# Performance work log

Hardware: AMD Instinct MI355X
Metric: run time of the kernel (lower is better)

The kernel has to match this reference:

```python
import jax, jax.numpy as jnp
import numpy as np

N_STREAMS = 4096


def setup_inputs() -> dict:
    key = jax.random.key(0)
    # Plain Gaussian (well-separated singular values; the polar factor math is
    # identical to the module's eye + 0.01*randn init, just a different point).
    H_raw = jax.random.normal(key, (N_STREAMS, N_STREAMS), dtype=jnp.float32)
    return {"H_raw": H_raw}


def reference(H_raw) -> jnp.ndarray:
    # OrthogonalMixing.forward: orthogonal polar factor of H_raw via thin SVD.
    U, s, Vh = jnp.linalg.svd(H_raw, full_matrices=False)
    return U @ Vh  # (s, s), satisfies H^T H = I
```

## Files before the change

kernel.cpp:

```cpp
#include <hip/hip_runtime.h>
#include <hip/hip_bf16.h>
#include <hip/hip_fp16.h>

#define NN 4096
#define NGROW 8
#define NPOL 2
#define NITER (NGROW + NPOL)
#define NPOW 12
#define NKT (NN / 64)
#define NTRI 136
#define PRESCALE 32.0f

using f16 = _Float16;
typedef __attribute__((ext_vector_type(4))) float f32x4;
typedef __attribute__((ext_vector_type(8))) f16 h16x8;

__device__ inline void gl_lds16(const void* g, void* l) {
  __builtin_amdgcn_global_load_lds(
      (const __attribute__((address_space(1))) unsigned int*)(unsigned long long)(uintptr_t)g,
      (__attribute__((address_space(3))) unsigned int*)(uintptr_t)l,
      16, 0, 0);
}

template <int EPI, int TRI>
__global__ __launch_bounds__(512, 2) void gemm_nt(
    const f16* __restrict__ P, const f16* __restrict__ Q,
    void* __restrict__ Out, const f16* __restrict__ aux,
    float alpha, float beta) {
  int bi, bj;
  if (TRI) {
    const int t = blockIdx.x;
    int r = (int)((sqrtf(8.0f * (float)t + 1.0f) - 1.0f) * 0.5f);
    while ((r + 1) * (r + 2) / 2 <= t) ++r;
    while (r * (r + 1) / 2 > t) --r;
    bi = r;
    bj = t - r * (r + 1) / 2;
  } else {
    bi = blockIdx.x;
    bj = blockIdx.y;
  }

  __shared__ f16 lA[2][256 * 64];
  __shared__ f16 lB[2][256 * 64];

  const int tid = threadIdx.x;
  const int lane = tid & 63;
  const int wv = tid >> 6;
  const int wr = wv >> 2;
  const int wc = wv & 3;
  const int m = lane & 15;
  const int qd = lane >> 4;
  const int srow = tid >> 3;
  const int schk = tid & 7;

  f32x4 acc[8][4] = {};

#define STAGE_A(u_, kk_, b_)                                                  \
  do {                                                                        \
    const int rr_ = (u_)*64 + srow;                                           \
    gl_lds16(P + (size_t)(bi * 256 + rr_) * NN + (kk_) + ((schk ^ (srow & 7)) * 8), \
             &lA[b_][(u_)*4096 + tid * 8]);                                   \
  } while (0)
#define STAGE_B(u_, kk_, b_)                                                  \
  do {                                                                        \
    const int rr_ = (u_)*64 + srow;                                           \
    gl_lds16(Q + (size_t)(bj * 256 + rr_) * NN + (kk_) + ((schk ^ (srow & 7)) * 8), \
             &lB[b_][(u_)*4096 + tid * 8]);                                   \
  } while (0)

#define READ_B_FR(b_)                                                         \
  do {                                                                        \
    _Pragma("unroll") for (int cf = 0; cf < 4; ++cf)                          \
    _Pragma("unroll") for (int ks = 0; ks < 2; ++ks) {                        \
      const int rb = wc * 64 + cf * 16 + m;                                   \
      const int cb = (ks * 4 + qd) ^ (rb & 7);                                \
      bv[cf][ks] = *(const h16x8*)&lB[b_][rb * 64 + cb * 8];                  \
    }                                                                         \
  } while (0)
#define READ_A_FR(b_, q_)                                                     \
  do {                                                                        \
    _Pragma("unroll") for (int rf = 0; rf < 2; ++rf)                          \
    _Pragma("unroll") for (int ks = 0; ks < 2; ++ks) {                        \
      const int ra = wr * 128 + (q_)*32 + rf * 16 + m;                        \
      const int ca = (ks * 4 + qd) ^ (ra & 7);                                \
      av[rf][ks] = *(const h16x8*)&lA[b_][ra * 64 + ca * 8];                  \
    }                                                                         \
  } while (0)
#define MFMA_Q(q_)                                                            \
  do {                                                                        \
    _Pragma("unroll") for (int rf = 0; rf < 2; ++rf)                          \
    _Pragma("unroll") for (int cf = 0; cf < 4; ++cf)                          \
    _Pragma("unroll") for (int ks = 0; ks < 2; ++ks)                          \
        acc[(q_)*2 + rf][cf] = __builtin_amdgcn_mfma_f32_16x16x32_f16(        \
            av[rf][ks], bv[cf][ks], acc[(q_)*2 + rf][cf], 0, 0, 0);           \
  } while (0)

#define BAR() __builtin_amdgcn_s_barrier()
#define PRIO(x_) __builtin_amdgcn_s_setprio(x_)
#define VMCNT(n_) asm volatile("s_waitcnt vmcnt(" #n_ ")" ::: "memory")
#define LGKM(n_) asm volatile("s_waitcnt lgkmcnt(" #n_ ")" ::: "memory")

#define TILE_STEADY(t_, b_, nb_)                                              \
  {                                                                           \
    const int k1 = ((t_) + 1) * 64, k2 = ((t_) + 2) * 64;                     \
    h16x8 av[2][2], bv[4][2];                                                 \
    READ_B_FR(b_);                                                            \
    READ_A_FR(b_, 0);                                                         \
    STAGE_A(1, k1, nb_); STAGE_A(3, k1, nb_);                                 \
    LGKM(8); BAR(); LGKM(0);                                                  \
    PRIO(1); MFMA_Q(0); PRIO(0);                                              \
    READ_A_FR(b_, 1);                                                         \
    STAGE_B(0, k2, b_); STAGE_B(1, k2, b_);                                   \
    BAR(); LGKM(0);                                                           \
    PRIO(1); MFMA_Q(1); PRIO(0);                                              \
    READ_A_FR(b_, 2);                                                         \
    STAGE_B(2, k2, b_); STAGE_B(3, k2, b_);                                   \
    BAR(); LGKM(0);                                                           \
    PRIO(1); MFMA_Q(2); PRIO(0);                                              \
    READ_A_FR(b_, 3);                                                         \
    STAGE_A(0, k2, b_); STAGE_A(2, k2, b_);                                   \
    BAR(); LGKM(0);                                                           \
    PRIO(1); MFMA_Q(3); PRIO(0);                                              \
    VMCNT(6); BAR();                                                          \
  }

  STAGE_B(0, 0, 0); STAGE_B(1, 0, 0); STAGE_B(2, 0, 0); STAGE_B(3, 0, 0);
  STAGE_A(0, 0, 0); STAGE_A(1, 0, 0); STAGE_A(2, 0, 0); STAGE_A(3, 0, 0);
  STAGE_B(0, 64, 1); STAGE_B(1, 64, 1); STAGE_B(2, 64, 1); STAGE_B(3, 64, 1);
  STAGE_A(0, 64, 1); STAGE_A(2, 64, 1);
  VMCNT(6);
  BAR();

  for (int tt = 0; tt < NKT - 2; tt += 2) {
    TILE_STEADY(tt, 0, 1);
    TILE_STEADY(tt + 1, 1, 0);
  }

  {
    h16x8 av[2][2], bv[4][2];
    READ_B_FR(0);
    READ_A_FR(0, 0);
    STAGE_A(1, (NKT - 1) * 64, 1); STAGE_A(3, (NKT - 1) * 64, 1);
    LGKM(8); BAR(); LGKM(0);
    PRIO(1); MFMA_Q(0); PRIO(0);
    READ_A_FR(0, 1);
    BAR(); LGKM(0);
    PRIO(1); MFMA_Q(1); PRIO(0);
    READ_A_FR(0, 2);
    BAR(); LGKM(0);
    PRIO(1); MFMA_Q(2); PRIO(0);
    READ_A_FR(0, 3);
    BAR(); LGKM(0);
    PRIO(1); MFMA_Q(3); PRIO(0);
    VMCNT(0); BAR();
  }
  {
    h16x8 av[2][2], bv[4][2];
    READ_B_FR(1);
    READ_A_FR(1, 0);
    LGKM(8); BAR(); LGKM(0);
    PRIO(1); MFMA_Q(0); PRIO(0);
    READ_A_FR(1, 1);
    BAR(); LGKM(0);
    PRIO(1); MFMA_Q(1); PRIO(0);
    READ_A_FR(1, 2);
    BAR(); LGKM(0);
    PRIO(1); MFMA_Q(2); PRIO(0);
    READ_A_FR(1, 3);
    BAR(); LGKM(0);
    PRIO(1); MFMA_Q(3); PRIO(0);
  }

#pragma unroll
  for (int fr = 0; fr < 8; ++fr) {
#pragma unroll
    for (int fc = 0; fc < 4; ++fc) {
#pragma unroll
      for (int rg = 0; rg < 4; ++rg) {
        const int lr = wr * 128 + fr * 16 + qd * 4 + rg;
        const int lc = wc * 64 + fc * 16 + m;
        const size_t idx = (size_t)(bi * 256 + lr) * NN + bj * 256 + lc;
        float v = beta * acc[fr][fc][rg];
        if (alpha != 0.0f) v += alpha * (float)aux[idx];
        if (EPI == 0)
          ((f16*)Out)[idx] = (f16)v;
        else
          ((float*)Out)[idx] = v;
        if (TRI && bi != bj) {
          const size_t idxT = (size_t)(bj * 256 + lc) * NN + bi * 256 + lr;
          ((f16*)Out)[idxT] = (f16)v;
        }
      }
    }
  }
#undef STAGE_A
#undef STAGE_B
#undef READ_B_FR
#undef READ_A_FR
#undef MFMA_Q
#undef TILE_STEADY
#undef BAR
#undef PRIO
#undef VMCNT
#undef LGKM
}

__global__ void transpose_h(const unsigned short* __restrict__ in,
                            unsigned short* __restrict__ out) {
  __shared__ unsigned short tile[64][65];
  const int tx = threadIdx.x & 63;
  const int ty = threadIdx.x >> 6;
  const int bx = blockIdx.x, by = blockIdx.y;
#pragma unroll
  for (int rr = 0; rr < 16; ++rr) {
    const int row = rr * 4 + ty;
    tile[row][tx] = in[(size_t)(by * 64 + row) * NN + bx * 64 + tx];
  }
  __syncthreads();
#pragma unroll
  for (int rr = 0; rr < 16; ++rr) {
    const int row = rr * 4 + ty;
    out[(size_t)(bx * 64 + row) * NN + by * 64 + tx] = tile[tx][row];
  }
}

__global__ __launch_bounds__(256) void powmv(const f16* __restrict__ A,
                                             const float* __restrict__ vin,
                                             const float* __restrict__ snin,
                                             float* __restrict__ vout,
                                             float* __restrict__ snout) {
  const float scale = rsqrtf(*snin);
  const int row = blockIdx.x * 4 + (threadIdx.x >> 6);
  const int lane = threadIdx.x & 63;
  const f16* arow = A + (size_t)row * NN;
  float acc = 0.0f;
#pragma unroll
  for (int p = 0; p < 8; ++p) {
    const int c = p * 512 + lane * 8;
    const h16x8 av = *(const h16x8*)(arow + c);
    const float4 w0 = *(const float4*)(vin + c);
    const float4 w1 = *(const float4*)(vin + c + 4);
    acc += (float)av[0] * w0.x + (float)av[1] * w0.y + (float)av[2] * w0.z +
           (float)av[3] * w0.w + (float)av[4] * w1.x + (float)av[5] * w1.y +
           (float)av[6] * w1.z + (float)av[7] * w1.w;
  }
  for (int off = 32; off; off >>= 1) acc += __shfl_down(acc, off, 64);
  if (lane == 0) {
    const float u = acc * scale;
    vout[row] = u;
    atomicAdd(snout, u * u);
  }
}

__global__ void init_pw(float* __restrict__ v0, float* __restrict__ slots) {
  const int t = threadIdx.x;
  if (t < 64) slots[t] = (t == 1) ? 1.0f : 0.0f;
  for (int i = t; i < NN; i += 256) {
    const unsigned h = (unsigned)i * 2654435761u;
    v0[i] = ((h >> 16) & 1) ? 0.015625f : -0.015625f;
  }
}

__global__ void reduce_sumsq(const float* __restrict__ h, float* __restrict__ slots) {
  float acc = 0.0f;
  const size_t total = (size_t)NN * NN;
  for (size_t i = (size_t)blockIdx.x * blockDim.x + threadIdx.x; i < total;
       i += (size_t)gridDim.x * blockDim.x) {
    const float v = h[i];
    acc += v * v;
  }
  for (int off = 32; off; off >>= 1) acc += __shfl_down(acc, off, 64);
  __shared__ float ws[4];
  const int lane = threadIdx.x & 63, wv = threadIdx.x >> 6;
  if (lane == 0) ws[wv] = acc;
  __syncthreads();
  if (threadIdx.x == 0) atomicAdd(&slots[0], ws[0] + ws[1] + ws[2] + ws[3]);
}

__global__ void scale_cast(const float* __restrict__ h, const float* __restrict__ slots,
                           f16* __restrict__ xb, int mode) {
  float inv = rsqrtf(slots[0]) * PRESCALE;
  if (mode) inv *= rsqrtf(1.10f * sqrtf(slots[1 + NPOW]));
  const size_t i = ((size_t)blockIdx.x * blockDim.x + threadIdx.x) * 4;
  const float4 v = *(const float4*)(h + i);
  union { f16 hh[4]; ushort4 u; } cvt;
  cvt.hh[0] = (f16)(v.x * inv);
  cvt.hh[1] = (f16)(v.y * inv);
  cvt.hh[2] = (f16)(v.z * inv);
  cvt.hh[3] = (f16)(v.w * inv);
  *(ushort4*)(xb + i) = cvt.u;
}

__global__ void rescale_f16(f16* __restrict__ a, const float* __restrict__ slots) {
  const float cA = 1.0f / (1.10f * sqrtf(slots[1 + NPOW]));
  const size_t i = ((size_t)blockIdx.x * 256 + threadIdx.x) * 8;
  h16x8 v = *(h16x8*)(a + i);
  h16x8 o;
#pragma unroll
  for (int j = 0; j < 8; ++j) o[j] = (f16)((float)v[j] * cA);
  *(h16x8*)(a + i) = o;
}

extern "C" void kernel_launch(void* const* d_in, const int* in_sizes, int n_in,
                              void* d_out, int out_size, void* d_ws, size_t ws_size,
                              hipStream_t stream) {
  (void)in_sizes; (void)n_in; (void)out_size; (void)ws_size;
  const float* H = (const float*)d_in[0];
  float* out = (float*)d_out;
  char* ws = (char*)d_ws;

  f16* P0 = (f16*)ws;
  f16* P1 = (f16*)(ws + ((size_t)32 << 20));
  f16* Ab = (f16*)(ws + ((size_t)64 << 20));
  f16* Bb = (f16*)((char*)d_out + ((size_t)32 << 20));
  float* v0 = (float*)d_out;
  float* v1 = (float*)((char*)d_out + 16384);
  float* slots = (float*)((char*)d_out + 32768);

  const dim3 gfull(16, 16), tbg(512), tb(256), gt(64, 64);

  init_pw<<<1, 256, 0, stream>>>(v0, slots);
  reduce_sumsq<<<1024, 256, 0, stream>>>(H, slots);
  scale_cast<<<(NN * (size_t)NN) / 4 / 256, 256, 0, stream>>>(H, slots, P0, 0);
  transpose_h<<<gt, tb, 0, stream>>>((const unsigned short*)P0, (unsigned short*)P1);
  gemm_nt<0, 1><<<NTRI, tbg, 0, stream>>>(P1, P1, Ab, (f16*)nullptr, 0.0f, 1.0f);
  for (int k = 0; k < NPOW; ++k) {
    const float* vi = (k & 1) ? v1 : v0;
    float* vo = (k & 1) ? v0 : v1;
    powmv<<<1024, 256, 0, stream>>>(Ab, vi, &slots[1 + k], vo, &slots[2 + k]);
  }
  rescale_f16<<<(NN * (size_t)NN) / 8 / 256, 256, 0, stream>>>(Ab, slots);
  scale_cast<<<(NN * (size_t)NN) / 4 / 256, 256, 0, stream>>>(H, slots, P0, 1);

  f16* X = P0;
  f16* Y = P1;
  const float GA = 3.4445f, GB = -4.7750f, GC = 2.0315f;
  const float PA = 1.875f, PB = -1.25f, PC = 0.375f;

  for (int it = 0; it < NITER; ++it) {
    const bool polish = it >= NGROW;
    const bool last = (it == NITER - 1);
    const float qa = polish ? PA : GA, qb = polish ? PB : GB, qc = polish ? PC : GC;

    if (it > 0) {
      transpose_h<<<gt, tb, 0, stream>>>((const unsigned short*)X, (unsigned short*)Y);
      gemm_nt<0, 1><<<NTRI, tbg, 0, stream>>>(Y, Y, Ab, (f16*)nullptr, 0.0f, 1.0f);
    }
    f16* Bdst = last ? Y : Bb;
    gemm_nt<0, 1><<<NTRI, tbg, 0, stream>>>(Ab, Ab, Bdst, Ab, qb, qc);
    if (!last) {
      gemm_nt<0, 0><<<gfull, tbg, 0, stream>>>(X, Bdst, Y, X, qa, 1.0f);
      f16* t = X; X = Y; Y = t;
    } else {
      gemm_nt<1, 0><<<gfull, tbg, 0, stream>>>(X, Bdst, out, X, qa, 1.0f);
    }
  }
}
```

Before: 4.708 ms.

## Software-pipeline LDS fragment reads with double-buffered registers and sched_group_barrier interleave

Restructures the GEMM main loop so the LDS fragment reads for the next quarter (and the next tile's B fragments) are issued while the current quarter's MFMAs run, using ping-pong register buffers for A and B. The explicit lgkmcnt waits and setprio calls are replaced by sched_group_barrier directives that interleave ds_reads, global-to-LDS loads and MFMAs. The goal is to hide LDS read latency behind matrix-core work instead of stalling before each MFMA block. In exchange it needs more VGPRs for the doubled fragment buffers, which may lower occupancy or cause spills, and it relies on the compiler honoring the schedule hints for correct waitcnt placement.

```diff
diff --git a/kernel.cpp b/kernel.cpp
--- a/kernel.cpp
+++ b/kernel.cpp
@@ -54,6 +54,8 @@
   const int schk = tid & 7;
 
   f32x4 acc[8][4] = {};
+  h16x8 avA[2][2], avB[2][2];
+  h16x8 bv0[4][2], bv1[4][2];
 
 #define STAGE_A(u_, kk_, b_)                                                  \
   do {                                                                        \
@@ -68,60 +70,77 @@
              &lB[b_][(u_)*4096 + tid * 8]);                                   \
   } while (0)
 
-#define READ_B_FR(b_)                                                         \
+#define READ_AV(dst_, b_, q_)                                                 \
+  do {                                                                        \
+    _Pragma("unroll") for (int rf = 0; rf < 2; ++rf)                          \
+    _Pragma("unroll") for (int ks = 0; ks < 2; ++ks) {                        \
+      const int ra = wr * 128 + (q_)*32 + rf * 16 + m;                        \
+      const int ca = (ks * 4 + qd) ^ (ra & 7);                                \
+      dst_[rf][ks] = *(const h16x8*)&lA[b_][ra * 64 + ca * 8];                \
+    }                                                                         \
+  } while (0)
+#define READ_BV(dst_, b_)                                                     \
   do {                                                                        \
     _Pragma("unroll") for (int cf = 0; cf < 4; ++cf)                          \
     _Pragma("unroll") for (int ks = 0; ks < 2; ++ks) {                        \
       const int rb = wc * 64 + cf * 16 + m;                                   \
       const int cb = (ks * 4 + qd) ^ (rb & 7);                                \
-      bv[cf][ks] = *(const h16x8*)&lB[b_][rb * 64 + cb * 8];                  \
+      dst_[cf][ks] = *(const h16x8*)&lB[b_][rb * 64 + cb * 8];                \
     }                                                                         \
   } while (0)
-#define READ_A_FR(b_, q_)                                                     \
-  do {                                                                        \
-    _Pragma("unroll") for (int rf = 0; rf < 2; ++rf)                          \
-    _Pragma("unroll") for (int ks = 0; ks < 2; ++ks) {                        \
-      const int ra = wr * 128 + (q_)*32 + rf * 16 + m;                        \
-      const int ca = (ks * 4 + qd) ^ (ra & 7);                                \
-      av[rf][ks] = *(const h16x8*)&lA[b_][ra * 64 + ca * 8];                  \
-    }                                                                         \
-  } while (0)
-#define MFMA_Q(q_)                                                            \
+#define MFMA_Q(q_, A_, B_)                                                    \
   do {                                                                        \
     _Pragma("unroll") for (int rf = 0; rf < 2; ++rf)                          \
     _Pragma("unroll") for (int cf = 0; cf < 4; ++cf)                          \
     _Pragma("unroll") for (int ks = 0; ks < 2; ++ks)                          \
         acc[(q_)*2 + rf][cf] = __builtin_amdgcn_mfma_f32_16x16x32_f16(        \
-            av[rf][ks], bv[cf][ks], acc[(q_)*2 + rf][cf], 0, 0, 0);           \
+            A_[rf][ks], B_[cf][ks], acc[(q_)*2 + rf][cf], 0, 0, 0);           \
   } while (0)
 
 #define BAR() __builtin_amdgcn_s_barrier()
-#define PRIO(x_) __builtin_amdgcn_s_setprio(x_)
 #define VMCNT(n_) asm volatile("s_waitcnt vmcnt(" #n_ ")" ::: "memory")
-#define LGKM(n_) asm volatile("s_waitcnt lgkmcnt(" #n_ ")" ::: "memory")
-
-#define TILE_STEADY(t_, b_, nb_)                                              \
+#define SGB(m_, n_) __builtin_amdgcn_sched_group_barrier(m_, n_, 0)
+#define SGB_RD4_ST2()                                                         \
+  do { SGB(0x8,2); SGB(0x100,1); SGB(0x8,2); SGB(0x100,1); SGB(0x8,2);        \
+       SGB(0x100,1); SGB(0x8,2); SGB(0x100,1); SGB(0x8,2); SGB(0x30,1);       \
+       SGB(0x8,3); SGB(0x30,1); SGB(0x8,3); } while (0)
+#define SGB_RD4_ST0()                                                         \
+  do { SGB(0x8,3); SGB(0x100,1); SGB(0x8,3); SGB(0x100,1); SGB(0x8,3);        \
+       SGB(0x100,1); SGB(0x8,3); SGB(0x100,1); SGB(0x8,4); } while (0)
+#define SGB_RD12_ST2()                                                        \
+  do { SGB(0x100,2); SGB(0x8,2); SGB(0x100,2); SGB(0x8,2); SGB(0x100,2);      \
+       SGB(0x8,2); SGB(0x100,2); SGB(0x8,2); SGB(0x100,2); SGB(0x8,2);        \
+       SGB(0x100,2); SGB(0x8,2); SGB(0x30,1); SGB(0x8,2); SGB(0x30,1);        \
+       SGB(0x8,2); } while (0)
+#define SGB_RD12_ST0()                                                        \
+  do { SGB(0x100,2); SGB(0x8,2); SGB(0x100,2); SGB(0x8,2); SGB(0x100,2);      \
+       SGB(0x8,2); SGB(0x100,2); SGB(0x8,2); SGB(0x100,2); SGB(0x8,2);        \
+       SGB(0x100,2); SGB(0x8,2); SGB(0x8,4); } while (0)
+
+#define TILE_STEADY(t_, b_, nb_, BVC_, BVN_)                                  \
   {                                                                           \
     const int k1 = ((t_) + 1) * 64, k2 = ((t_) + 2) * 64;                     \
-    h16x8 av[2][2], bv[4][2];                                                 \
-    READ_B_FR(b_);                                                            \
-    READ_A_FR(b_, 0);                                                         \
+                                                                      \
+    READ_AV(avB, b_, 1);                                                      \
     STAGE_A(1, k1, nb_); STAGE_A(3, k1, nb_);                                 \
-    LGKM(8); BAR(); LGKM(0);                                                  \
-    PRIO(1); MFMA_Q(0); PRIO(0);                                              \
-    READ_A_FR(b_, 1);                                                         \
+    MFMA_Q(0, avA, BVC_);                                                     \
+    SGB_RD4_ST2(); BAR();                                                     \
+                                                                      \
+    READ_AV(avA, b_, 2);                                                      \
     STAGE_B(0, k2, b_); STAGE_B(1, k2, b_);                                   \
-    BAR(); LGKM(0);                                                           \
-    PRIO(1); MFMA_Q(1); PRIO(0);                                              \
-    READ_A_FR(b_, 2);                                                         \
+    MFMA_Q(1, avB, BVC_);                                                     \
+    SGB_RD4_ST2(); BAR();                                                     \
+                                                                      \
+    READ_AV(avB, b_, 3);                                                      \
     STAGE_B(2, k2, b_); STAGE_B(3, k2, b_);                                   \
-    BAR(); LGKM(0);                                                           \
-    PRIO(1); MFMA_Q(2); PRIO(0);                                              \
-    READ_A_FR(b_, 3);                                                         \
+    MFMA_Q(2, avA, BVC_);                                                     \
+    SGB_RD4_ST2(); VMCNT(4); BAR();                                           \
+                 \
+    READ_BV(BVN_, nb_);                                                       \
+    READ_AV(avA, nb_, 0);                                                     \
     STAGE_A(0, k2, b_); STAGE_A(2, k2, b_);                                   \
-    BAR(); LGKM(0);                                                           \
-    PRIO(1); MFMA_Q(3); PRIO(0);                                              \
-    VMCNT(6); BAR();                                                          \
+    MFMA_Q(3, avB, BVC_);                                                     \
+    SGB_RD12_ST2(); BAR();                                                    \
   }
 
   STAGE_B(0, 0, 0); STAGE_B(1, 0, 0); STAGE_B(2, 0, 0); STAGE_B(3, 0, 0);
@@ -130,45 +149,42 @@
   STAGE_A(0, 64, 1); STAGE_A(2, 64, 1);
   VMCNT(6);
   BAR();
+  READ_BV(bv0, 0);
+  READ_AV(avA, 0, 0);
+  BAR();
 
   for (int tt = 0; tt < NKT - 2; tt += 2) {
-    TILE_STEADY(tt, 0, 1);
-    TILE_STEADY(tt + 1, 1, 0);
+    TILE_STEADY(tt, 0, 1, bv0, bv1);
+    TILE_STEADY(tt + 1, 1, 0, bv1, bv0);
   }
 
   {
-    h16x8 av[2][2], bv[4][2];
-    READ_B_FR(0);
-    READ_A_FR(0, 0);
+    READ_AV(avB, 0, 1);
     STAGE_A(1, (NKT - 1) * 64, 1); STAGE_A(3, (NKT - 1) * 64, 1);
-    LGKM(8); BAR(); LGKM(0);
-    PRIO(1); MFMA_Q(0); PRIO(0);
-    READ_A_FR(0, 1);
-    BAR(); LGKM(0);
-    PRIO(1); MFMA_Q(1); PRIO(0);
-    READ_A_FR(0, 2);
-    BAR(); LGKM(0);
-    PRIO(1); MFMA_Q(2); PRIO(0);
-    READ_A_FR(0, 3);
-    BAR(); LGKM(0);
-    PRIO(1); MFMA_Q(3); PRIO(0);
-    VMCNT(0); BAR();
+    MFMA_Q(0, avA, bv0);
+    SGB_RD4_ST2(); BAR();
+    READ_AV(avA, 0, 2);
+    MFMA_Q(1, avB, bv0);
+    SGB_RD4_ST0(); BAR();
+    READ_AV(avB, 0, 3);
+    MFMA_Q(2, avA, bv0);
+    SGB_RD4_ST0(); VMCNT(0); BAR();
+    READ_BV(bv1, 1);
+    READ_AV(avA, 1, 0);
+    MFMA_Q(3, avB, bv0);
+    SGB_RD12_ST0(); BAR();
   }
   {
-    h16x8 av[2][2], bv[4][2];
-    READ_B_FR(1);
-    READ_A_FR(1, 0);
-    LGKM(8); BAR(); LGKM(0);
-    PRIO(1); MFMA_Q(0); PRIO(0);
-    READ_A_FR(1, 1);
-    BAR(); LGKM(0);
-    PRIO(1); MFMA_Q(1); PRIO(0);
-    READ_A_FR(1, 2);
-    BAR(); LGKM(0);
-    PRIO(1); MFMA_Q(2); PRIO(0);
-    READ_A_FR(1, 3);
-    BAR(); LGKM(0);
-    PRIO(1); MFMA_Q(3); PRIO(0);
+    READ_AV(avB, 1, 1);
+    MFMA_Q(0, avA, bv1);
+    SGB_RD4_ST0(); BAR();
+    READ_AV(avA, 1, 2);
+    MFMA_Q(1, avB, bv1);
+    SGB_RD4_ST0(); BAR();
+    READ_AV(avB, 1, 3);
+    MFMA_Q(2, avA, bv1);
+    SGB_RD4_ST0(); BAR();
+    MFMA_Q(3, avB, bv1);
   }
 
 #pragma unroll
@@ -195,14 +211,17 @@
   }
 #undef STAGE_A
 #undef STAGE_B
-#undef READ_B_FR
-#undef READ_A_FR
+#undef READ_AV
+#undef READ_BV
 #undef MFMA_Q
 #undef TILE_STEADY
 #undef BAR
-#undef PRIO
 #undef VMCNT
-#undef LGKM
+#undef SGB
+#undef SGB_RD4_ST2
+#undef SGB_RD4_ST0
+#undef SGB_RD12_ST2
+#undef SGB_RD12_ST0
 }
 
 __global__ void transpose_h(const unsigned short* __restrict__ in,
```

Measured after the change: 4.454 ms. -5.4%, faster.
